# Kernel optimization log

Measured on AMD Instinct MI355X. Metric: run time of the kernel, lower is better.

Reference implementation:

```python
import jax, jax.numpy as jnp
import numpy as np
from jax.scipy.special import logsumexp

NEG = -1e9  # stands in for log(0) = -inf in the padded one-hots (avoids NaN-producing -inf)


def setup_inputs() -> dict:
    key = jax.random.key(0)
    ks = jax.random.split(key, 9)
    Lx, Ly, B, D, Vout = 64, 64, 128, 256, 53
    return {
        "prior_ctx": jax.random.normal(ks[0], (Lx, B, D), dtype=jnp.float32),
        "modern_ctx": jax.random.normal(ks[1], (Ly, B, D), dtype=jnp.float32),
        "W_sub": jax.random.normal(ks[2], (Vout, D), dtype=jnp.float32) * 0.05,
        "b_sub": jax.random.normal(ks[3], (Vout,), dtype=jnp.float32) * 0.05,
        "W_ins": jax.random.normal(ks[4], (Vout, D), dtype=jnp.float32) * 0.05,
        "b_ins": jax.random.normal(ks[5], (Vout,), dtype=jnp.float32) * 0.05,
        "target_ids": jax.random.randint(ks[6], (Ly - 1, B), 0, Vout, dtype=jnp.int32),
        "src_lengths": jax.random.randint(ks[7], (B,), 1, Lx + 1),
        "tgt_lengths": jax.random.randint(ks[8], (B,), 1, Ly + 1),
    }


def reference(prior_ctx, modern_ctx, W_sub, b_sub, W_ins, b_ins,
              target_ids, src_lengths, tgt_lengths):
    Lx, B, D = prior_ctx.shape
    Ly = modern_ctx.shape[0]
    Vout = W_sub.shape[0]

    # outer-sum context: [Lx, Ly, B, D]
    ctx = prior_ctx[:, None, :, :] + modern_ctx[None, :, :, :]

    # padding matrix: True where both source pos i and target pos j are valid. [Lx, Ly, B, 1]
    mask = ((jnp.arange(Lx)[:, None, None] < src_lengths[None, None, :])
            & (jnp.arange(Ly)[None, :, None] < tgt_lengths[None, None, :]))[..., None]

    # heads: Linear + LogSoftmax, zeroed on padding. [Lx, Ly, B, Vout]
    sub = jnp.where(mask, jax.nn.log_softmax(jnp.einsum('xybd,vd->xybv', ctx, W_sub) + b_sub, axis=-1), 0.0)
    ins = jnp.where(mask, jax.nn.log_softmax(jnp.einsum('xybd,vd->xybv', ctx, W_ins) + b_ins, axis=-1), 0.0)

    del_probs = sub[:, :, :, Vout - 1]  # [Lx, Ly, B]
    end_probs = ins[:, :, :, Vout - 1]

    # log one-hots of targets shifted by 1: [Ly-1, B, Vout]
    log_oh = jnp.where(target_ids[:, :, None] == jnp.arange(Vout)[None, None, :], 0.0, NEG)

    sub_probs = logsumexp(sub[:, :-1] + log_oh[None], axis=-1)  # [Lx, Ly-1, B]
    ins_probs = logsumexp(ins[:, :-1] + log_oh[None], axis=-1)
    return del_probs, end_probs, sub_probs, ins_probs
```

## Files before the change

kernel.cpp:

```cpp
#include <hip/hip_runtime.h>

#define D   256
#define NB  128
#define NV  53
#define NR  8192
#define V4  14
#define SLB (V4*NR*4)
#define ESOFF (4*SLB)
#define WBOFF (8*SLB)
#define BTOFF (WBOFF + 3584*8)
#define A52   (13*NR*4)
#define LOG2E 1.44269504088896340736f
#define LN2   0.69314718055994530942f


typedef float  f4 __attribute__((ext_vector_type(4)));
typedef float  f2 __attribute__((ext_vector_type(2)));
typedef short  s8 __attribute__((ext_vector_type(8)));

__device__ __forceinline__ ushort f2bf(float f) {
    uint u = __float_as_uint(f);
    u += 0x7fff + ((u >> 16) & 1);
    return (ushort)(u >> 16);
}
__device__ __forceinline__ float bflo(uint w) { return __uint_as_float(w << 16); }
__device__ __forceinline__ float bfhi(uint w) { return __uint_as_float(w & 0xffff0000u); }
__device__ __forceinline__ float fexp2(float x) { return __builtin_exp2f(x); }
__device__ __forceinline__ float flog2(float x) { return __builtin_log2f(x); }

__global__ void p0_kernel(const float* __restrict__ Wsub, const float* __restrict__ Wins,
                          const float* __restrict__ bsub, const float* __restrict__ bins,
                          ushort* __restrict__ WBg, float* __restrict__ biasT)
{
    const int F  = blockIdx.x * 64 + threadIdx.x;
    const int l  = F & 63, s = (F >> 6) & 7, nt = F >> 9;
    const int o  = nt * 16 + (l & 15);
    const int d0 = 32 * s + 8 * (l >> 4);
    const float* w = nullptr;
    if (o < NV)       w = Wsub + o * D + d0;
    else if (o < 106) w = Wins + (o - NV) * D + d0;
    s8 bfr;
    if (w) {
        #pragma unroll
        for (int j = 0; j < 8; ++j) bfr[j] = (short)f2bf(w[j] * LOG2E);
    } else {
        #pragma unroll
        for (int j = 0; j < 8; ++j) bfr[j] = 0;
    }
    *(s8*)&WBg[F * 8] = bfr;
    if (F < 112) {
        float bv = 0.f;
        if (F < NV)       bv = bsub[F] * LOG2E;
        else if (F < 106) bv = bins[F - NV] * LOG2E;
        biasT[F] = bv;
    }
}

__global__ __launch_bounds__(256) void p1_kernel(
    const float* __restrict__ prior, const float* __restrict__ modern,
    const ushort* __restrict__ WBg, const float* __restrict__ biasT,
    ushort* __restrict__ wsb)
{
    __shared__ ushort WB[3584 * 8];
    const int tid = threadIdx.x;

    #pragma unroll
    for (int i = 0; i < 14; ++i) {
        const int idx = i * 256 + tid;
        *(s8*)&WB[idx * 8] = *(const s8*)&WBg[idx * 8];
    }
    __syncthreads();

    const int wave = tid >> 6, lane = tid & 63;
    const int tile = blockIdx.x * 4 + wave;
    const int side = tile >> 9;
    const int row0 = (tile & 511) << 4;
    const int lrow = lane & 15, lk = lane >> 4;
    const float* __restrict__ src =
        (side ? modern : prior) + (size_t)(row0 + lrow) * D + lk * 8;

    f4 c[16];
    #pragma unroll
    for (int s = 0; s < 8; ++s) {
        c[2*s]   = *(const f4*)(src + 32 * s);
        c[2*s+1] = *(const f4*)(src + 32 * s + 4);
    }

    f4 acc[7];
    #pragma unroll
    for (int nt = 0; nt < 7; ++nt) { acc[nt][0]=0.f; acc[nt][1]=0.f; acc[nt][2]=0.f; acc[nt][3]=0.f; }

    #pragma unroll
    for (int s = 0; s < 8; ++s) {
        s8 a;
        a[0]=(short)f2bf(c[2*s][0]); a[1]=(short)f2bf(c[2*s][1]);
        a[2]=(short)f2bf(c[2*s][2]); a[3]=(short)f2bf(c[2*s][3]);
        a[4]=(short)f2bf(c[2*s+1][0]); a[5]=(short)f2bf(c[2*s+1][1]);
        a[6]=(short)f2bf(c[2*s+1][2]); a[7]=(short)f2bf(c[2*s+1][3]);
        #pragma unroll
        for (int nt = 0; nt < 7; ++nt) {
            const s8 bfr = *(const s8*)&WB[(((nt << 3) + s) * 64 + lane) * 8];
            acc[nt] = __builtin_amdgcn_mfma_f32_16x16x32_bf16(a, bfr, acc[nt], 0, 0, 0);
        }
    }

    #pragma unroll
    for (int nt = 0; nt < 7; ++nt) {
        const int v = nt * 16 + lrow;
        if (v < 106) {
            const bool isS = v < NV;
            const int  vi  = isS ? v : v - NV;
            const float bias = side ? biasT[v] : 0.f;
            ushort* __restrict__ raw = wsb + (size_t)(side * 2 + (isS ? 0 : 1)) * SLB;
            ushort* __restrict__ Eb  = raw + ESOFF;
            const int a0 = (vi >> 2) * (NR * 4) + (vi & 3);
            #pragma unroll
            for (int r = 0; r < 4; ++r) {
                const int row = row0 + 4 * lk + r;
                const float val = acc[nt][r] + bias;
                raw[a0 + row * 4] = f2bf(val);
                Eb[a0 + row * 4]  = f2bf(fexp2(val));
            }
        }
    }
    if (lrow >= 10 && lrow <= 12) {
        const int vi = 43 + lrow;
        const int a0 = (vi >> 2) * (NR * 4) + (vi & 3);
        #pragma unroll
        for (int r = 0; r < 4; ++r) {
            const int row = row0 + 4 * lk + r;
            wsb[ESOFF + (size_t)(side * 2 + 0) * SLB + a0 + row * 4] = 0;
            wsb[ESOFF + (size_t)(side * 2 + 1) * SLB + a0 + row * 4] = 0;
        }
    }
}

__global__ __launch_bounds__(256) void p2_kernel(
    const ushort* __restrict__ wsb,
    const int* __restrict__ target, const int* __restrict__ srclen,
    const int* __restrict__ tgtlen, float* __restrict__ out)
{
    const int tid = threadIdx.x;
    const int b   = tid & 127;
    const int bid = blockIdx.x;
    const int xt  = ((bid & 7) << 1) | ((bid >> 3) & 1);
    const int y   = ((bid >> 4) << 1) | (tid >> 7);
    const int yb  = y * NB + b;

    const int sl = srclen[b], tl = tgtlen[b];
    const bool ymask = y < tl;
    const bool hasT  = y < 63;
    const int  t     = hasT ? target[y * NB + b] : 0;
    const int  toff  = (t >> 2) * (NR * 4) + (t & 3);

    #pragma unroll 1
    for (int dist = 0; dist < 2; ++dist) {
        const ushort* __restrict__ Praw = wsb + dist * SLB;
        const ushort* __restrict__ Mraw = wsb + (2 + dist) * SLB;
        const ushort* __restrict__ PE   = Praw + ESOFF;
        const ushort* __restrict__ ME   = Mraw + ESOFF;

        f2 em0[V4], em1[V4];
        #pragma unroll
        for (int g = 0; g < V4; ++g) {
            const uint2 q = *(const uint2*)(ME + (g * NR + yb) * 4);
            em0[g][0] = bflo(q.x); em0[g][1] = bfhi(q.x);
            em1[g][0] = bflo(q.y); em1[g][1] = bfhi(q.y);
        }
        const float mlt = bflo((uint)Mraw[toff + yb * 4]);
        const float m52 = bflo((uint)Mraw[A52  + yb * 4]);

        float* __restrict__ o0 = out + dist * 524288;
        float* __restrict__ o1 = out + 1048576 + dist * 516096;

        #pragma unroll
        for (int xi = 0; xi < 4; ++xi) {
            const int x  = (xt << 2) + xi;
            const int xb = x * NB + b;
            const bool msk = (x < sl) & ymask;

            f2 s0; s0[0] = 0.f; s0[1] = 0.f;
            f2 s1; s1[0] = 0.f; s1[1] = 0.f;
            #pragma unroll
            for (int g = 0; g < V4; ++g) {
                const uint2 p = *(const uint2*)(PE + (g * NR + xb) * 4);
                f2 a; a[0] = bflo(p.x); a[1] = bfhi(p.x);
                f2 c; c[0] = bflo(p.y); c[1] = bfhi(p.y);
                s0 += a * em0[g];
                s1 += c * em1[g];
            }
            const float S  = (s0[0] + s0[1]) + (s1[0] + s1[1]);
            const float ls = flog2(S);

            const float l52 = bflo((uint)Praw[A52 + xb * 4]) + m52;
            o0[((x << 6) | y) * NB + b] = msk ? (l52 - ls) * LN2 : 0.f;
            if (hasT) {
                const float lt = bflo((uint)Praw[toff + xb * 4]) + mlt;
                o1[(x * 63 + y) * NB + b] = msk ? (lt - ls) * LN2 : 0.f;
            }
        }
    }
}

extern "C" void kernel_launch(void* const* d_in, const int* in_sizes, int n_in,
                              void* d_out, int out_size, void* d_ws, size_t ws_size,
                              hipStream_t stream) {
    const float* prior  = (const float*)d_in[0];
    const float* modern = (const float*)d_in[1];
    const float* Wsub   = (const float*)d_in[2];
    const float* bsub   = (const float*)d_in[3];
    const float* Wins   = (const float*)d_in[4];
    const float* bins   = (const float*)d_in[5];
    const int*   target = (const int*)d_in[6];
    const int*   srclen = (const int*)d_in[7];
    const int*   tgtlen = (const int*)d_in[8];
    ushort* wsb   = (ushort*)d_ws;
    ushort* WBg   = wsb + WBOFF;
    float*  biasT = (float*)(wsb + BTOFF);
    float*  out   = (float*)d_out;

    p0_kernel<<<56, 64, 0, stream>>>(Wsub, Wins, bsub, bins, WBg, biasT);
    p1_kernel<<<256, 256, 0, stream>>>(prior, modern, WBg, biasT, wsb);
    p2_kernel<<<512, 256, 0, stream>>>(wsb, target, srclen, tgtlen, out);
}
```

Measured before the change: 38.35 us.

## Fuse weight prep into projection kernel and shrink tiles for more blocks

Removes the separate weight-conversion kernel: each projection block now loads fp32 weights, converts them to bf16 and writes them into an XOR-swizzled shared-memory layout, and reads the bias directly. Projection waves now handle 8 rows instead of 16, so the grid doubles. Half the MFMA lanes are wasted on duplicated rows and every block repeats the weight conversion. The pairwise kernel now gives each block 2 x positions instead of 4 and launches twice as many blocks, trading fewer launches and more parallelism for extra redundant loads of the modern-side exponentials.

```diff
diff --git a/kernel.cpp b/kernel.cpp
--- a/kernel.cpp
+++ b/kernel.cpp
@@ -7,8 +7,6 @@
 #define V4  14
 #define SLB (V4*NR*4)
 #define ESOFF (4*SLB)
-#define WBOFF (8*SLB)
-#define BTOFF (WBOFF + 3584*8)
 #define A52   (13*NR*4)
 #define LOG2E 1.44269504088896340736f
 #define LN2   0.69314718055994530942f
@@ -28,56 +26,46 @@
 __device__ __forceinline__ float fexp2(float x) { return __builtin_exp2f(x); }
 __device__ __forceinline__ float flog2(float x) { return __builtin_log2f(x); }
 
-__global__ void p0_kernel(const float* __restrict__ Wsub, const float* __restrict__ Wins,
-                          const float* __restrict__ bsub, const float* __restrict__ bins,
-                          ushort* __restrict__ WBg, float* __restrict__ biasT)
-{
-    const int F  = blockIdx.x * 64 + threadIdx.x;
-    const int l  = F & 63, s = (F >> 6) & 7, nt = F >> 9;
-    const int o  = nt * 16 + (l & 15);
-    const int d0 = 32 * s + 8 * (l >> 4);
-    const float* w = nullptr;
-    if (o < NV)       w = Wsub + o * D + d0;
-    else if (o < 106) w = Wins + (o - NV) * D + d0;
-    s8 bfr;
-    if (w) {
-        #pragma unroll
-        for (int j = 0; j < 8; ++j) bfr[j] = (short)f2bf(w[j] * LOG2E);
-    } else {
-        #pragma unroll
-        for (int j = 0; j < 8; ++j) bfr[j] = 0;
-    }
-    *(s8*)&WBg[F * 8] = bfr;
-    if (F < 112) {
-        float bv = 0.f;
-        if (F < NV)       bv = bsub[F] * LOG2E;
-        else if (F < 106) bv = bins[F - NV] * LOG2E;
-        biasT[F] = bv;
-    }
-}
-
 __global__ __launch_bounds__(256) void p1_kernel(
     const float* __restrict__ prior, const float* __restrict__ modern,
-    const ushort* __restrict__ WBg, const float* __restrict__ biasT,
+    const float* __restrict__ Wsub, const float* __restrict__ bsub,
+    const float* __restrict__ Wins, const float* __restrict__ bins,
     ushort* __restrict__ wsb)
 {
-    __shared__ ushort WB[3584 * 8];
+    __shared__ ushort WL[112 * 256];
     const int tid = threadIdx.x;
 
     #pragma unroll
-    for (int i = 0; i < 14; ++i) {
-        const int idx = i * 256 + tid;
-        *(s8*)&WB[idx * 8] = *(const s8*)&WBg[idx * 8];
+    for (int j = 0; j < 14; ++j) {
+        const int t  = j * 256 + tid;
+        const int o  = t >> 5, ch = t & 31;
+        const float* w = nullptr;
+        if (o < NV)       w = Wsub + o * D + ch * 8;
+        else if (o < 106) w = Wins + (o - NV) * D + ch * 8;
+        s8 q;
+        if (w) {
+            const f4 a = *(const f4*)w;
+            const f4 b = *(const f4*)(w + 4);
+            q[0]=(short)f2bf(a[0]*LOG2E); q[1]=(short)f2bf(a[1]*LOG2E);
+            q[2]=(short)f2bf(a[2]*LOG2E); q[3]=(short)f2bf(a[3]*LOG2E);
+            q[4]=(short)f2bf(b[0]*LOG2E); q[5]=(short)f2bf(b[1]*LOG2E);
+            q[6]=(short)f2bf(b[2]*LOG2E); q[7]=(short)f2bf(b[3]*LOG2E);
+        } else {
+            #pragma unroll
+            for (int i = 0; i < 8; ++i) q[i] = 0;
+        }
+        const int byteoff = o * 512 + ((ch * 16) ^ ((o & 7) << 4));
+        *(s8*)((char*)WL + byteoff) = q;
     }
     __syncthreads();
 
     const int wave = tid >> 6, lane = tid & 63;
-    const int tile = blockIdx.x * 4 + wave;
-    const int side = tile >> 9;
-    const int row0 = (tile & 511) << 4;
     const int lrow = lane & 15, lk = lane >> 4;
+    const int tile8 = blockIdx.x * 4 + wave;
+    const int side  = tile8 >> 10;
+    const int row0  = (tile8 & 1023) << 3;
     const float* __restrict__ src =
-        (side ? modern : prior) + (size_t)(row0 + lrow) * D + lk * 8;
+        (side ? modern : prior) + (size_t)(row0 + (lrow & 7)) * D + lk * 8;
 
     f4 c[16];
     #pragma unroll
@@ -90,47 +78,52 @@
     #pragma unroll
     for (int nt = 0; nt < 7; ++nt) { acc[nt][0]=0.f; acc[nt][1]=0.f; acc[nt][2]=0.f; acc[nt][3]=0.f; }
 
+    const int swzc = (lrow & 7) << 4;
     #pragma unroll
     for (int s = 0; s < 8; ++s) {
         s8 a;
-        a[0]=(short)f2bf(c[2*s][0]); a[1]=(short)f2bf(c[2*s][1]);
-        a[2]=(short)f2bf(c[2*s][2]); a[3]=(short)f2bf(c[2*s][3]);
+        a[0]=(short)f2bf(c[2*s][0]);   a[1]=(short)f2bf(c[2*s][1]);
+        a[2]=(short)f2bf(c[2*s][2]);   a[3]=(short)f2bf(c[2*s][3]);
         a[4]=(short)f2bf(c[2*s+1][0]); a[5]=(short)f2bf(c[2*s+1][1]);
         a[6]=(short)f2bf(c[2*s+1][2]); a[7]=(short)f2bf(c[2*s+1][3]);
         #pragma unroll
         for (int nt = 0; nt < 7; ++nt) {
-            const s8 bfr = *(const s8*)&WB[(((nt << 3) + s) * 64 + lane) * 8];
+            const int byte = (nt * 16 + lrow) * 512 + ((s * 64 + lk * 16) ^ swzc);
+            const s8 bfr = *(const s8*)((const char*)WL + byte);
             acc[nt] = __builtin_amdgcn_mfma_f32_16x16x32_bf16(a, bfr, acc[nt], 0, 0, 0);
         }
     }
 
-    #pragma unroll
-    for (int nt = 0; nt < 7; ++nt) {
-        const int v = nt * 16 + lrow;
-        if (v < 106) {
-            const bool isS = v < NV;
-            const int  vi  = isS ? v : v - NV;
-            const float bias = side ? biasT[v] : 0.f;
-            ushort* __restrict__ raw = wsb + (size_t)(side * 2 + (isS ? 0 : 1)) * SLB;
-            ushort* __restrict__ Eb  = raw + ESOFF;
+    if (lk < 2) {
+        #pragma unroll
+        for (int nt = 0; nt < 7; ++nt) {
+            const int v = nt * 16 + lrow;
+            if (v < 106) {
+                const bool isS = v < NV;
+                const int  vi  = isS ? v : v - NV;
+                float bias = 0.f;
+                if (side) bias = (isS ? bsub[v] : bins[v - NV]) * LOG2E;
+                ushort* __restrict__ raw = wsb + (size_t)(side * 2 + (isS ? 0 : 1)) * SLB;
+                ushort* __restrict__ Eb  = raw + ESOFF;
+                const int a0 = (vi >> 2) * (NR * 4) + (vi & 3);
+                #pragma unroll
+                for (int r = 0; r < 4; ++r) {
+                    const int row = row0 + 4 * lk + r;
+                    const float val = acc[nt][r] + bias;
+                    raw[a0 + row * 4] = f2bf(val);
+                    Eb[a0 + row * 4]  = f2bf(fexp2(val));
+                }
+            }
+        }
+        if (lrow >= 10 && lrow <= 12) {
+            const int vi = 43 + lrow;
             const int a0 = (vi >> 2) * (NR * 4) + (vi & 3);
             #pragma unroll
             for (int r = 0; r < 4; ++r) {
                 const int row = row0 + 4 * lk + r;
-                const float val = acc[nt][r] + bias;
-                raw[a0 + row * 4] = f2bf(val);
-                Eb[a0 + row * 4]  = f2bf(fexp2(val));
-            }
-        }
-    }
-    if (lrow >= 10 && lrow <= 12) {
-        const int vi = 43 + lrow;
-        const int a0 = (vi >> 2) * (NR * 4) + (vi & 3);
-        #pragma unroll
-        for (int r = 0; r < 4; ++r) {
-            const int row = row0 + 4 * lk + r;
-            wsb[ESOFF + (size_t)(side * 2 + 0) * SLB + a0 + row * 4] = 0;
-            wsb[ESOFF + (size_t)(side * 2 + 1) * SLB + a0 + row * 4] = 0;
+                wsb[ESOFF + (size_t)(side * 2 + 0) * SLB + a0 + row * 4] = 0;
+                wsb[ESOFF + (size_t)(side * 2 + 1) * SLB + a0 + row * 4] = 0;
+            }
         }
     }
 }
@@ -143,8 +136,8 @@
     const int tid = threadIdx.x;
     const int b   = tid & 127;
     const int bid = blockIdx.x;
-    const int xt  = ((bid & 7) << 1) | ((bid >> 3) & 1);
-    const int y   = ((bid >> 4) << 1) | (tid >> 7);
+    const int xt  = bid & 31;
+    const int y   = ((bid >> 5) << 1) | (tid >> 7);
     const int yb  = y * NB + b;
 
     const int sl = srclen[b], tl = tgtlen[b];
@@ -174,8 +167,8 @@
         float* __restrict__ o1 = out + 1048576 + dist * 516096;
 
         #pragma unroll
-        for (int xi = 0; xi < 4; ++xi) {
-            const int x  = (xt << 2) + xi;
+        for (int xi = 0; xi < 2; ++xi) {
+            const int x  = (xt << 1) + xi;
             const int xb = x * NB + b;
             const bool msk = (x < sl) & ymask;
 
@@ -214,12 +207,9 @@
     const int*   target = (const int*)d_in[6];
     const int*   srclen = (const int*)d_in[7];
     const int*   tgtlen = (const int*)d_in[8];
-    ushort* wsb   = (ushort*)d_ws;
-    ushort* WBg   = wsb + WBOFF;
-    float*  biasT = (float*)(wsb + BTOFF);
-    float*  out   = (float*)d_out;
-
-    p0_kernel<<<56, 64, 0, stream>>>(Wsub, Wins, bsub, bins, WBg, biasT);
-    p1_kernel<<<256, 256, 0, stream>>>(prior, modern, WBg, biasT, wsb);
-    p2_kernel<<<512, 256, 0, stream>>>(wsb, target, srclen, tgtlen, out);
-}
+    ushort* wsb = (ushort*)d_ws;
+    float*  out = (float*)d_out;
+
+    p1_kernel<<<512, 256, 0, stream>>>(prior, modern, Wsub, bsub, Wins, bins, wsb);
+    p2_kernel<<<1024, 256, 0, stream>>>(wsb, target, srclen, tgtlen, out);
+}
```

Result: slower. 43.62 us (+13.7%).
